# Kernel optimization log

Hardware: AMD Instinct MI355X
Metric: run time of the kernel (lower is better)

The kernel has to match this reference:

```python
import jax, jax.numpy as jnp
import numpy as np

B, H, W = 32, 56, 56
C_IN, C_OUT, GROUPS, K = 256, 256, 32, 3
EPS = 1e-5


def setup_inputs() -> dict:
    key = jax.random.key(0)
    k1, k2 = jax.random.split(key, 2)
    x = jax.random.normal(k1, (B, H, W, C_IN), dtype=jnp.float32)
    # HWIO grouped-conv kernel: I = C_IN // GROUPS = 8; equivalent to the
    # concatenation of the 32 per-group [3,3,8,8] Conv2d kernels along O.
    w = jax.random.normal(k2, (K, K, C_IN // GROUPS, C_OUT), dtype=jnp.float32) * 0.05
    b = jnp.zeros((C_OUT,), dtype=jnp.float32)
    gamma = jnp.ones((C_OUT,), dtype=jnp.float32)
    beta = jnp.zeros((C_OUT,), dtype=jnp.float32)
    return {"x": x, "w": w, "b": b, "gamma": gamma, "beta": beta}


def reference(x, w, b, gamma, beta):
    # Grouped conv: same math as tf.split -> per-group Conv2d -> tf.concat,
    # expressed as one native grouped convolution (feature_group_count).
    y = jax.lax.conv_general_dilated(
        x, w,
        window_strides=(1, 1),
        padding="SAME",
        dimension_numbers=("NHWC", "HWIO", "NHWC"),
        feature_group_count=GROUPS,
    ) + b  # [B,H,W,C_OUT]
    # BatchNorm (training forward: batch statistics over N,H,W per channel)
    mean = jnp.mean(y, axis=(0, 1, 2))
    var = jnp.var(y, axis=(0, 1, 2))
    y = (y - mean) * jax.lax.rsqrt(var + EPS) * gamma + beta
    # Act('relu')
    return jax.nn.relu(y)
```

## Files before the change

kernel.cpp:

```cpp
#include <hip/hip_runtime.h>
#include <hip/hip_bf16.h>

#define BB 32
#define HH 56
#define WW 56
#define CC 256
#define NPIX (BB*HH*WW)
#define GRP 32
#define GSZ (NPIX*8)
#define EPS 1e-5f

typedef short bf16x8 __attribute__((ext_vector_type(8)));
typedef float f32x4  __attribute__((ext_vector_type(4)));

__device__ __forceinline__ unsigned short f2bf(float f) {
    __hip_bfloat16 h = __float2bfloat16(f);
    return *reinterpret_cast<unsigned short*>(&h);
}


__global__ __launch_bounds__(256) void k_pre(
    const float* __restrict__ x, const float* __restrict__ wgt,
    __hip_bfloat16* __restrict__ xg, unsigned short* __restrict__ wT,
    float* __restrict__ stats)
{
    __shared__ unsigned short lx[32*260];
    const int t  = threadIdx.x;
    const int P0 = blockIdx.x * 32;

    if (blockIdx.x == 0) {
        if (t < 128)
            *(float4*)(stats + t*4) = make_float4(0.f, 0.f, 0.f, 0.f);
        const int cw = t;
        unsigned short* dst = wT + (size_t)cw*80;
        #pragma unroll
        for (int tap = 0; tap < 9; ++tap) {
            ushort4 s4;
            s4.x = f2bf(wgt[(tap*8+0)*CC + cw]);
            s4.y = f2bf(wgt[(tap*8+1)*CC + cw]);
            s4.z = f2bf(wgt[(tap*8+2)*CC + cw]);
            s4.w = f2bf(wgt[(tap*8+3)*CC + cw]);
            *(ushort4*)(dst + tap*8) = s4;
            s4.x = f2bf(wgt[(tap*8+4)*CC + cw]);
            s4.y = f2bf(wgt[(tap*8+5)*CC + cw]);
            s4.z = f2bf(wgt[(tap*8+6)*CC + cw]);
            s4.w = f2bf(wgt[(tap*8+7)*CC + cw]);
            *(ushort4*)(dst + tap*8 + 4) = s4;
        }
    }

    #pragma unroll
    for (int r = 0; r < 8; ++r) {
        const int id  = r*256 + t;
        const int pix = id >> 6;
        const int c4  = id & 63;
        float4 v = *(const float4*)(x + (size_t)(P0+pix)*CC + c4*4);
        ushort4 s;
        s.x = f2bf(v.x); s.y = f2bf(v.y); s.z = f2bf(v.z); s.w = f2bf(v.w);
        *(ushort4*)(lx + pix*260 + c4*4) = s;
    }
    __syncthreads();
    #pragma unroll
    for (int r = 0; r < 4; ++r) {
        const int oid = r*256 + t;
        const int pl  = oid & 31;
        const int g   = oid >> 5;
        ushort4 a = *(const ushort4*)(lx + pl*260 + g*8);
        ushort4 c = *(const ushort4*)(lx + pl*260 + g*8 + 4);
        __hip_bfloat16* dst = xg + (size_t)g*GSZ + (size_t)(P0+pl)*8;
        *(ushort4*)dst       = a;
        *(ushort4*)(dst + 4) = c;
    }
}

__global__ __launch_bounds__(256, 8) void k1_conv(
    const __hip_bfloat16* __restrict__ xg, const unsigned short* __restrict__ wT,
    __hip_bfloat16* __restrict__ yg, float* __restrict__ stats)
{
    __shared__ unsigned short xt[10*58*16];
    __shared__ float bsum[16], bsq[16];

    const int gp = blockIdx.x;
    const int hb = blockIdx.y;
    const int b  = blockIdx.z;
    const int t  = threadIdx.x;
    const int h0 = hb * 8;

    if (t < 16) { bsum[t] = 0.f; bsq[t] = 0.f; }

    const int lane = t & 63;
    const int rp   = t >> 6;
    const int n    = lane & 15;
    const int q    = lane >> 4;

    const unsigned short* wrow = wT + (size_t)(gp*16 + n)*80;
    bf16x8 wfrag[5];
    #pragma unroll
    for (int s = 0; s < 5; ++s) {
        const int o   = s*4 + q;
        const int g   = (o >= 10);
        const int tap = o - g*10;
        bf16x8 f = {0,0,0,0,0,0,0,0};
        if (tap < 9 && (n >> 3) == g)
            f = *(const bf16x8*)(wrow + tap*8);
        wfrag[s] = f;
    }

    #pragma unroll
    for (int j = 0; j < 5; ++j) {
        const int e   = j*256 + t;
        const int col = e % 58;
        const int rg  = e / 58;
        const int row = rg >> 1;
        const int g   = rg & 1;
        const int hh  = h0 - 1 + row;
        const int wc  = col - 1;
        uint4 v = make_uint4(0u, 0u, 0u, 0u);
        if (e < 1160 && (unsigned)hh < HH && (unsigned)wc < WW)
            v = *(const uint4*)(xg + (size_t)(gp*2+g)*GSZ
                                   + (size_t)((b*HH + hh)*WW + wc)*8);
        if (e < 1160)
            *(uint4*)(xt + (row*58 + col)*16 + g*8) = v;
    }

    __syncthreads();

    const int m    = lane & 15;
    const int rowr = rp*2 + (m >> 3);
    const int colb = m & 7;

    int aoff[5];
    #pragma unroll
    for (int s = 0; s < 5; ++s) {
        int o  = s*4 + q;
        int g  = (o >= 10);
        int tp = o - g*10;
        if (tp == 9) tp = 0;
        int dh = tp / 3, dw = tp - dh*3;
        aoff[s] = ((rowr + dh)*58 + colb + dw)*16 + g*8;
    }

    const int h = h0 + rowr;
    const size_t pixbase = ((size_t)(b*HH + h))*WW;
    float lsum[4] = {0.f, 0.f, 0.f, 0.f};
    float lsq[4]  = {0.f, 0.f, 0.f, 0.f};

    #pragma unroll 2
    for (int ct = 0; ct < 7; ++ct) {
        f32x4 acc = {0.f, 0.f, 0.f, 0.f};
        #pragma unroll
        for (int s = 0; s < 5; ++s) {
            bf16x8 af = *(const bf16x8*)(xt + aoff[s] + ct*128);
            acc = __builtin_amdgcn_mfma_f32_16x16x32_bf16(wfrag[s], af, acc, 0, 0, 0);
        }
        ushort4 st;
        st.x = f2bf(acc[0]); st.y = f2bf(acc[1]);
        st.z = f2bf(acc[2]); st.w = f2bf(acc[3]);
        *(ushort4*)(yg + ((size_t)gp*NPIX + pixbase + ct*8 + colb)*16 + q*4) = st;
        #pragma unroll
        for (int i = 0; i < 4; ++i) {
            lsum[i] += acc[i];
            lsq[i]  += acc[i]*acc[i];
        }
    }

    #pragma unroll
    for (int d = 8; d >= 1; d >>= 1) {
        #pragma unroll
        for (int i = 0; i < 4; ++i) {
            lsum[i] += __shfl_xor(lsum[i], d);
            lsq[i]  += __shfl_xor(lsq[i],  d);
        }
    }
    if (m == 0) {
        #pragma unroll
        for (int i = 0; i < 4; ++i) {
            atomicAdd(&bsum[q*4 + i], lsum[i]);
            atomicAdd(&bsq[q*4 + i],  lsq[i]);
        }
    }
    __syncthreads();
    if (t < 16) {
        atomicAdd(&stats[gp*16 + t],       bsum[t]);
        atomicAdd(&stats[256 + gp*16 + t], bsq[t]);
    }
}

__global__ __launch_bounds__(256) void k3_norm(
    const __hip_bfloat16* __restrict__ yg, const float* __restrict__ stats,
    const float* __restrict__ gamma, const float* __restrict__ beta,
    float* __restrict__ out)
{
    __shared__ unsigned short lx[32*260];
    const int t  = threadIdx.x;
    const int P0 = blockIdx.x * 32;

    #pragma unroll
    for (int r = 0; r < 2; ++r) {
        const int id = r*256 + t;
        const int g  = id >> 5;
        const int pl = id & 31;
        const __hip_bfloat16* src = yg + ((size_t)g*NPIX + P0 + pl)*16;
        uint4 v0 = *(const uint4*)(src);
        uint4 v1 = *(const uint4*)(src + 8);
        *(uint4*)(lx + pl*260 + g*16)     = v0;
        *(uint4*)(lx + pl*260 + g*16 + 8) = v1;
    }

    const int oct = t & 31;
    const int pr  = t >> 5;
    const int c0  = oct * 8;
    const float inv_n = 1.f / (float)NPIX;
    float sc[8], sh[8];
    #pragma unroll
    for (int i = 0; i < 8; ++i) {
        float mean = stats[c0+i] * inv_n;
        float var  = stats[256+c0+i] * inv_n - mean*mean;
        float s    = gamma[c0+i] * rsqrtf(var + EPS);
        sc[i] = s;
        sh[i] = beta[c0+i] - mean * s;
    }
    __syncthreads();

    #pragma unroll
    for (int i = 0; i < 4; ++i) {
        const int pl = pr + i*8;
        ushort4 a = *(const ushort4*)(lx + pl*260 + c0);
        ushort4 c = *(const ushort4*)(lx + pl*260 + c0 + 4);
        float f0 = __uint_as_float((unsigned)a.x << 16);
        float f1 = __uint_as_float((unsigned)a.y << 16);
        float f2 = __uint_as_float((unsigned)a.z << 16);
        float f3 = __uint_as_float((unsigned)a.w << 16);
        float f4 = __uint_as_float((unsigned)c.x << 16);
        float f5 = __uint_as_float((unsigned)c.y << 16);
        float f6 = __uint_as_float((unsigned)c.z << 16);
        float f7 = __uint_as_float((unsigned)c.w << 16);

        float4 o0, o1;
        o0.x = fmaxf(0.f, f0 * sc[0] + sh[0]);
        o0.y = fmaxf(0.f, f1 * sc[1] + sh[1]);
        o0.z = fmaxf(0.f, f2 * sc[2] + sh[2]);
        o0.w = fmaxf(0.f, f3 * sc[3] + sh[3]);
        o1.x = fmaxf(0.f, f4 * sc[4] + sh[4]);
        o1.y = fmaxf(0.f, f5 * sc[5] + sh[5]);
        o1.z = fmaxf(0.f, f6 * sc[6] + sh[6]);
        o1.w = fmaxf(0.f, f7 * sc[7] + sh[7]);

        float* dst = out + (size_t)(P0 + pl)*CC + c0;
        *(float4*)(dst)     = o0;
        *(float4*)(dst + 4) = o1;
    }
}

extern "C" void kernel_launch(void* const* d_in, const int* in_sizes, int n_in,
                              void* d_out, int out_size, void* d_ws, size_t ws_size,
                              hipStream_t stream) {
    const float* x     = (const float*)d_in[0];
    const float* wgt   = (const float*)d_in[1];
    const float* gamma = (const float*)d_in[3];
    const float* beta  = (const float*)d_in[4];
    float* out = (float*)d_out;

    float* stats = (float*)d_ws;
    __hip_bfloat16* yg = (__hip_bfloat16*)((char*)d_ws + 4096);
    __hip_bfloat16* xg = (__hip_bfloat16*)((char*)d_ws + 4096 + (size_t)NPIX*CC*2);
    unsigned short* wT = (unsigned short*)((char*)d_ws + 4096 + 2*(size_t)NPIX*CC*2);

    k_pre<<<NPIX/32, 256, 0, stream>>>(x, wgt, xg, wT, stats);
    k1_conv<<<dim3(16, 7, BB), 256, 0, stream>>>(xg, wT, yg, stats);
    k3_norm<<<NPIX/32, 256, 0, stream>>>(yg, stats, gamma, beta, out);
}
```

Baseline: 233.1 us.

## Fuse fp32-to-bf16 input conversion into conv kernel with 8x8 spatial patches

Removes the pre-pass that converted x to bf16 and re-laid it out per group. The conv kernel now loads fp32 NHWC directly for a 10x10 halo patch across all 256 channels, converts to bf16 in LDS, and has each wave process four groups. This drops a full read and write of an intermediate bf16 tensor. In exchange it spends more LDS per block (lower occupancy, launch bounds 3), recomputes about 56% of the halo loads, and issues more global atomics for stats.

```diff
diff --git a/kernel.cpp b/kernel.cpp
--- a/kernel.cpp
+++ b/kernel.cpp
@@ -6,8 +6,6 @@
 #define WW 56
 #define CC 256
 #define NPIX (BB*HH*WW)
-#define GRP 32
-#define GSZ (NPIX*8)
 #define EPS 1e-5f
 
 typedef short bf16x8 __attribute__((ext_vector_type(8)));
@@ -19,115 +17,65 @@
 }
 
 
-__global__ __launch_bounds__(256) void k_pre(
-    const float* __restrict__ x, const float* __restrict__ wgt,
-    __hip_bfloat16* __restrict__ xg, unsigned short* __restrict__ wT,
+__global__ __launch_bounds__(256) void k_init(
+    const float* __restrict__ wgt, unsigned short* __restrict__ wT,
     float* __restrict__ stats)
 {
-    __shared__ unsigned short lx[32*260];
-    const int t  = threadIdx.x;
-    const int P0 = blockIdx.x * 32;
-
-    if (blockIdx.x == 0) {
-        if (t < 128)
-            *(float4*)(stats + t*4) = make_float4(0.f, 0.f, 0.f, 0.f);
-        const int cw = t;
-        unsigned short* dst = wT + (size_t)cw*80;
-        #pragma unroll
-        for (int tap = 0; tap < 9; ++tap) {
-            ushort4 s4;
-            s4.x = f2bf(wgt[(tap*8+0)*CC + cw]);
-            s4.y = f2bf(wgt[(tap*8+1)*CC + cw]);
-            s4.z = f2bf(wgt[(tap*8+2)*CC + cw]);
-            s4.w = f2bf(wgt[(tap*8+3)*CC + cw]);
-            *(ushort4*)(dst + tap*8) = s4;
-            s4.x = f2bf(wgt[(tap*8+4)*CC + cw]);
-            s4.y = f2bf(wgt[(tap*8+5)*CC + cw]);
-            s4.z = f2bf(wgt[(tap*8+6)*CC + cw]);
-            s4.w = f2bf(wgt[(tap*8+7)*CC + cw]);
-            *(ushort4*)(dst + tap*8 + 4) = s4;
-        }
-    }
-
-    #pragma unroll
-    for (int r = 0; r < 8; ++r) {
+    const int t = threadIdx.x;
+    if (t < 128)
+        *(float4*)(stats + t*4) = make_float4(0.f, 0.f, 0.f, 0.f);
+    const int cw = t;
+    unsigned short* dst = wT + (size_t)cw*80;
+    #pragma unroll
+    for (int tap = 0; tap < 9; ++tap) {
+        ushort4 s4;
+        s4.x = f2bf(wgt[(tap*8+0)*CC + cw]);
+        s4.y = f2bf(wgt[(tap*8+1)*CC + cw]);
+        s4.z = f2bf(wgt[(tap*8+2)*CC + cw]);
+        s4.w = f2bf(wgt[(tap*8+3)*CC + cw]);
+        *(ushort4*)(dst + tap*8) = s4;
+        s4.x = f2bf(wgt[(tap*8+4)*CC + cw]);
+        s4.y = f2bf(wgt[(tap*8+5)*CC + cw]);
+        s4.z = f2bf(wgt[(tap*8+6)*CC + cw]);
+        s4.w = f2bf(wgt[(tap*8+7)*CC + cw]);
+        *(ushort4*)(dst + tap*8 + 4) = s4;
+    }
+}
+
+__global__ __launch_bounds__(256, 3) void k1_conv(
+    const float* __restrict__ x, const unsigned short* __restrict__ wT,
+    __hip_bfloat16* __restrict__ yg, float* __restrict__ stats)
+{
+    __shared__ unsigned short xt[16*1608];
+    const int patch = blockIdx.x;
+    const int b     = blockIdx.y;
+    const int t     = threadIdx.x;
+    const int ph    = patch / 7, pw = patch - ph*7;
+    const int h0    = ph * 8,    w0 = pw * 8;
+
+    #pragma unroll 5
+    for (int r = 0; r < 25; ++r) {
         const int id  = r*256 + t;
-        const int pix = id >> 6;
+        const int rec = id >> 6;
         const int c4  = id & 63;
-        float4 v = *(const float4*)(x + (size_t)(P0+pix)*CC + c4*4);
+        const int pr_ = rec / 10;
+        const int pc_ = rec - pr_*10;
+        const int hh  = h0 - 1 + pr_;
+        const int wc  = w0 - 1 + pc_;
+        float4 v = make_float4(0.f, 0.f, 0.f, 0.f);
+        if ((unsigned)hh < HH && (unsigned)wc < WW)
+            v = *(const float4*)(x + ((size_t)(b*HH + hh)*WW + wc)*CC + c4*4);
         ushort4 s;
         s.x = f2bf(v.x); s.y = f2bf(v.y); s.z = f2bf(v.z); s.w = f2bf(v.w);
-        *(ushort4*)(lx + pix*260 + c4*4) = s;
-    }
-    __syncthreads();
-    #pragma unroll
-    for (int r = 0; r < 4; ++r) {
-        const int oid = r*256 + t;
-        const int pl  = oid & 31;
-        const int g   = oid >> 5;
-        ushort4 a = *(const ushort4*)(lx + pl*260 + g*8);
-        ushort4 c = *(const ushort4*)(lx + pl*260 + g*8 + 4);
-        __hip_bfloat16* dst = xg + (size_t)g*GSZ + (size_t)(P0+pl)*8;
-        *(ushort4*)dst       = a;
-        *(ushort4*)(dst + 4) = c;
-    }
-}
-
-__global__ __launch_bounds__(256, 8) void k1_conv(
-    const __hip_bfloat16* __restrict__ xg, const unsigned short* __restrict__ wT,
-    __hip_bfloat16* __restrict__ yg, float* __restrict__ stats)
-{
-    __shared__ unsigned short xt[10*58*16];
-    __shared__ float bsum[16], bsq[16];
-
-    const int gp = blockIdx.x;
-    const int hb = blockIdx.y;
-    const int b  = blockIdx.z;
-    const int t  = threadIdx.x;
-    const int h0 = hb * 8;
-
-    if (t < 16) { bsum[t] = 0.f; bsq[t] = 0.f; }
+        *(ushort4*)(xt + (c4>>2)*1608 + rec*16 + (c4&3)*4) = s;
+    }
 
     const int lane = t & 63;
-    const int rp   = t >> 6;
-    const int n    = lane & 15;
+    const int w    = t >> 6;
+    const int m    = lane & 15;
     const int q    = lane >> 4;
-
-    const unsigned short* wrow = wT + (size_t)(gp*16 + n)*80;
-    bf16x8 wfrag[5];
-    #pragma unroll
-    for (int s = 0; s < 5; ++s) {
-        const int o   = s*4 + q;
-        const int g   = (o >= 10);
-        const int tap = o - g*10;
-        bf16x8 f = {0,0,0,0,0,0,0,0};
-        if (tap < 9 && (n >> 3) == g)
-            f = *(const bf16x8*)(wrow + tap*8);
-        wfrag[s] = f;
-    }
-
-    #pragma unroll
-    for (int j = 0; j < 5; ++j) {
-        const int e   = j*256 + t;
-        const int col = e % 58;
-        const int rg  = e / 58;
-        const int row = rg >> 1;
-        const int g   = rg & 1;
-        const int hh  = h0 - 1 + row;
-        const int wc  = col - 1;
-        uint4 v = make_uint4(0u, 0u, 0u, 0u);
-        if (e < 1160 && (unsigned)hh < HH && (unsigned)wc < WW)
-            v = *(const uint4*)(xg + (size_t)(gp*2+g)*GSZ
-                                   + (size_t)((b*HH + hh)*WW + wc)*8);
-        if (e < 1160)
-            *(uint4*)(xt + (row*58 + col)*16 + g*8) = v;
-    }
-
-    __syncthreads();
-
-    const int m    = lane & 15;
-    const int rowr = rp*2 + (m >> 3);
     const int colb = m & 7;
+    const int prow = m >> 3;
 
     int aoff[5];
     #pragma unroll
@@ -137,52 +85,64 @@
         int tp = o - g*10;
         if (tp == 9) tp = 0;
         int dh = tp / 3, dw = tp - dh*3;
-        aoff[s] = ((rowr + dh)*58 + colb + dw)*16 + g*8;
-    }
-
-    const int h = h0 + rowr;
-    const size_t pixbase = ((size_t)(b*HH + h))*WW;
-    float lsum[4] = {0.f, 0.f, 0.f, 0.f};
-    float lsq[4]  = {0.f, 0.f, 0.f, 0.f};
-
-    #pragma unroll 2
-    for (int ct = 0; ct < 7; ++ct) {
-        f32x4 acc = {0.f, 0.f, 0.f, 0.f};
+        aoff[s] = ((prow + dh)*10 + colb + dw)*16 + g*8;
+    }
+
+    __syncthreads();
+
+    #pragma unroll
+    for (int gi = 0; gi < 4; ++gi) {
+        const int gp = w*4 + gi;
+        const unsigned short* wrow = wT + (size_t)(gp*16 + m)*80;
+        bf16x8 wfrag[5];
         #pragma unroll
         for (int s = 0; s < 5; ++s) {
-            bf16x8 af = *(const bf16x8*)(xt + aoff[s] + ct*128);
-            acc = __builtin_amdgcn_mfma_f32_16x16x32_bf16(wfrag[s], af, acc, 0, 0, 0);
-        }
-        ushort4 st;
-        st.x = f2bf(acc[0]); st.y = f2bf(acc[1]);
-        st.z = f2bf(acc[2]); st.w = f2bf(acc[3]);
-        *(ushort4*)(yg + ((size_t)gp*NPIX + pixbase + ct*8 + colb)*16 + q*4) = st;
+            const int o   = s*4 + q;
+            const int g   = (o >= 10);
+            const int tap = o - g*10;
+            bf16x8 f = {0,0,0,0,0,0,0,0};
+            if (tap < 9 && (m >> 3) == g)
+                f = *(const bf16x8*)(wrow + tap*8);
+            wfrag[s] = f;
+        }
+        const int sbase = gp*1608;
+        float lsum[4] = {0.f,0.f,0.f,0.f};
+        float lsq[4]  = {0.f,0.f,0.f,0.f};
+
         #pragma unroll
-        for (int i = 0; i < 4; ++i) {
-            lsum[i] += acc[i];
-            lsq[i]  += acc[i]*acc[i];
-        }
-    }
-
-    #pragma unroll
-    for (int d = 8; d >= 1; d >>= 1) {
+        for (int pt = 0; pt < 4; ++pt) {
+            f32x4 acc = {0.f,0.f,0.f,0.f};
+            #pragma unroll
+            for (int s = 0; s < 5; ++s) {
+                bf16x8 af = *(const bf16x8*)(xt + sbase + aoff[s] + pt*320);
+                acc = __builtin_amdgcn_mfma_f32_16x16x32_bf16(wfrag[s], af, acc, 0, 0, 0);
+            }
+            const int pix = (b*HH + h0 + pt*2 + prow)*WW + w0 + colb;
+            ushort4 st;
+            st.x = f2bf(acc[0]); st.y = f2bf(acc[1]);
+            st.z = f2bf(acc[2]); st.w = f2bf(acc[3]);
+            *(ushort4*)(yg + ((size_t)gp*NPIX + pix)*16 + q*4) = st;
+            #pragma unroll
+            for (int i = 0; i < 4; ++i) {
+                lsum[i] += acc[i];
+                lsq[i]  += acc[i]*acc[i];
+            }
+        }
         #pragma unroll
-        for (int i = 0; i < 4; ++i) {
-            lsum[i] += __shfl_xor(lsum[i], d);
-            lsq[i]  += __shfl_xor(lsq[i],  d);
-        }
-    }
-    if (m == 0) {
-        #pragma unroll
-        for (int i = 0; i < 4; ++i) {
-            atomicAdd(&bsum[q*4 + i], lsum[i]);
-            atomicAdd(&bsq[q*4 + i],  lsq[i]);
-        }
-    }
-    __syncthreads();
-    if (t < 16) {
-        atomicAdd(&stats[gp*16 + t],       bsum[t]);
-        atomicAdd(&stats[256 + gp*16 + t], bsq[t]);
+        for (int d = 8; d >= 1; d >>= 1) {
+            #pragma unroll
+            for (int i = 0; i < 4; ++i) {
+                lsum[i] += __shfl_xor(lsum[i], d);
+                lsq[i]  += __shfl_xor(lsq[i],  d);
+            }
+        }
+        if (m == 0) {
+            #pragma unroll
+            for (int i = 0; i < 4; ++i) {
+                atomicAdd(&stats[gp*16 + q*4 + i],       lsum[i]);
+                atomicAdd(&stats[256 + gp*16 + q*4 + i], lsq[i]);
+            }
+        }
     }
 }
 
@@ -263,10 +223,9 @@
 
     float* stats = (float*)d_ws;
     __hip_bfloat16* yg = (__hip_bfloat16*)((char*)d_ws + 4096);
-    __hip_bfloat16* xg = (__hip_bfloat16*)((char*)d_ws + 4096 + (size_t)NPIX*CC*2);
-    unsigned short* wT = (unsigned short*)((char*)d_ws + 4096 + 2*(size_t)NPIX*CC*2);
-
-    k_pre<<<NPIX/32, 256, 0, stream>>>(x, wgt, xg, wT, stats);
-    k1_conv<<<dim3(16, 7, BB), 256, 0, stream>>>(xg, wT, yg, stats);
+    unsigned short* wT = (unsigned short*)((char*)d_ws + 4096 + (size_t)NPIX*CC*2);
+
+    k_init<<<1, 256, 0, stream>>>(wgt, wT, stats);
+    k1_conv<<<dim3(49, BB), 256, 0, stream>>>(x, wT, yg, stats);
     k3_norm<<<NPIX/32, 256, 0, stream>>>(yg, stats, gamma, beta, out);
 }
```

Result: slower. 368.2 us (+57.9%).
